# Kernel optimization log

Measured on AMD Instinct MI355X. Metric: run time of the kernel, lower is better.

## Reference

```python
import jax, jax.numpy as jnp
import numpy as np

N_PIECES = 20  # hard-coded in FSEncoderSized.__init__ (FSPool(..., 20))


def conv1x1(x, w, b):
    # x: (B, Cin, N), w: (Cout, Cin), b: (Cout,) -> (B, Cout, N)
    return jnp.einsum('bcn,dc->bdn', x, w) + b[None, :, None]


def fspool(x, weight):
    # x: (B, C, N); weight: (C, N_PIECES+1)
    # FSPool with n=None: sizes = arange(N)/(N-1) clamped to 1, mask all ones.
    B, C, N = x.shape
    ratio = jnp.clip(jnp.arange(N, dtype=jnp.float32) / max(N - 1, 1), 0.0, 1.0)
    pos = N_PIECES * ratio                      # (N,) in [0, N_PIECES]
    idx = jnp.floor(pos).astype(jnp.int32)
    frac = pos - idx
    left = weight[:, idx]                       # (C, N)
    right = weight[:, jnp.clip(idx + 1, 0, N_PIECES)]
    w = (1.0 - frac)[None, :] * left + frac[None, :] * right  # (C, N)
    xs = -jnp.sort(-x, axis=2)                  # descending sort along set dim
    return jnp.sum(xs * w[None], axis=2)        # (B, C)


def setup_inputs() -> dict:
    key = jax.random.key(0)
    ks = jax.random.split(key, 12)
    B, Cin, N = 1024, 5, 512
    dim, Cout = 256, 129
    C = Cout - 1  # 128
    x = jax.random.normal(ks[0], (B, Cin, N), dtype=jnp.float32)
    mask = (jax.random.uniform(ks[1], (B, N)) < 0.8).astype(jnp.float32)

    def kaiming(k, co, ci):
        return jax.random.normal(k, (co, ci), dtype=jnp.float32) * np.sqrt(2.0 / ci)

    w1 = kaiming(ks[2], dim, Cin); b1 = jnp.zeros((dim,), jnp.float32)
    w2 = kaiming(ks[3], dim, dim); b2 = jnp.zeros((dim,), jnp.float32)
    w3 = kaiming(ks[4], dim, dim); b3 = jnp.zeros((dim,), jnp.float32)
    w4 = kaiming(ks[5], C, dim);   b4 = jnp.zeros((C,), jnp.float32)
    pool_w = jax.random.normal(ks[6], (C, N_PIECES + 1), dtype=jnp.float32) * 0.1
    return {'x': x, 'mask': mask, 'w1': w1, 'b1': b1, 'w2': w2, 'b2': b2,
            'w3': w3, 'b3': b3, 'w4': w4, 'b4': b4, 'pool_w': pool_w}


def reference(x, mask, w1, b1, w2, b2, w3, b3, w4, b4, pool_w):
    m = mask[:, None, :]                         # (B, 1, N)
    h = jax.nn.relu(conv1x1(x, w1, b1))
    h = jax.nn.relu(conv1x1(h, w2, b2))
    h = jax.nn.relu(conv1x1(h, w3, b3))
    h = conv1x1(h, w4, b4)                       # (B, C, N)
    h = h / h.shape[2]                           # x / x.size(2)
    h = h * m
    pooled = fspool(h, pool_w)                   # (B, C)
    size_feat = jnp.mean(m, axis=2) * 4.0        # (B, 1)
    return jnp.concatenate([pooled, size_feat], axis=1)  # (B, C+1)
```

## Files before the change

### kernel.cpp

```cpp
#include <hip/hip_runtime.h>
#include <hip/hip_bf16.h>

typedef __bf16 bf16x8 __attribute__((ext_vector_type(8)));
typedef float f32x4 __attribute__((ext_vector_type(4)));
typedef unsigned short ushort_t;

#define NPOS 512
#define CIN  5
#define CO   128

static __device__ __forceinline__ unsigned short f2bf(float f){
  union { __hip_bfloat16 h; unsigned short u; } cv;
  cv.h = __float2bfloat16(f);
  return cv.u;
}

static __device__ __forceinline__ unsigned cvtpk_u32(float a, float b){
  union { __hip_bfloat162 h2; unsigned u; } cv;
  cv.h2 = __float22bfloat162_rn(make_float2(a, b));
  return cv.u;
}

static __device__ __forceinline__ unsigned pk_min_u16(unsigned a, unsigned b){
  unsigned d; asm("v_pk_min_u16 %0, %1, %2" : "=v"(d) : "v"(a), "v"(b)); return d;
}
static __device__ __forceinline__ unsigned pk_max_u16(unsigned a, unsigned b){
  unsigned d; asm("v_pk_max_u16 %0, %1, %2" : "=v"(d) : "v"(a), "v"(b)); return d;
}
static __device__ __forceinline__ unsigned pk_max_i16(unsigned a, unsigned b){
  unsigned d; asm("v_pk_max_i16 %0, %1, %2" : "=v"(d) : "v"(a), "v"(b)); return d;
}

template<int CTRL>
static __device__ __forceinline__ unsigned mov_dpp_u32(unsigned v){
  return (unsigned)__builtin_amdgcn_mov_dpp((int)v, CTRL, 0xf, 0xf, true);
}
template<int CTRL>
static __device__ __forceinline__ float fadd_dpp(float s){
  union {float f; int i;} u; u.f = s;
  union {int i; float f;} q; q.i = __builtin_amdgcn_mov_dpp(u.i, CTRL, 0xf, 0xf, true);
  return s + q.f;
}

__global__ void k_prep(const float* __restrict__ w1, const float* __restrict__ w2,
                       const float* __restrict__ w3, const float* __restrict__ w4,
                       const float* __restrict__ pw,
                       ushort_t* __restrict__ o, float* __restrict__ Wt){
  int i = blockIdx.x*256 + threadIdx.x;
  if (i < 65536)        o[i] = f2bf(w2[i]);
  else if (i < 131072)  o[i] = f2bf(w3[i-65536]);
  else if (i < 163840)  o[i] = f2bf(w4[i-131072]);
  else if (i < 172032){
    int j = i - 163840;
    int d = j >> 5, k = j & 31;
    o[i] = (k < CIN) ? f2bf(w1[d*CIN + k]) : (ushort_t)0;
  } else {
    int j = i - 172032;
    int c = j >> 9, ii = j & 511;
    int rk = 511 - ii;
    float pos = (float)rk * (20.0f/511.0f);
    int idx = (int)pos; if (idx > 20) idx = 20;
    float frac = pos - (float)idx;
    int i2 = (idx+1 > 20) ? 20 : idx+1;
    float wl = pw[c*21 + idx], wr = pw[c*21 + i2];
    Wt[c*512 + ii] = wl + frac*(wr - wl);
  }
}


template<int NSD, int KSTR>
static __device__ __forceinline__ void preload_w(bf16x8 (&wr)[3][4],
    const ushort_t* __restrict__ Wb, int slot, int ks, int wave, int lane){
  const int m = lane & 15, quad = lane >> 4;
  const int d0 = wave * (NSD*16);
  #pragma unroll
  for (int sd=0; sd<NSD; sd++)
    wr[slot][sd] = *(const bf16x8*)(Wb + (d0 + sd*16 + m)*KSTR + ks*32 + quad*8);
}

template<int NKS>
static __device__ __forceinline__ void mfma_WA(bf16x8 (&wr)[3][4],
    const ushort_t* __restrict__ Wb,
    const ushort_t* __restrict__ A0, const ushort_t* __restrict__ A1,
    const float* __restrict__ bias,
    f32x4 (&c0)[4][4], f32x4 (&c1)[4][4], int wave, int lane){
  const int quad = lane >> 4;
  f32x4 bvv[4];
  #pragma unroll
  for (int db=0; db<4; db++){
    float4 b4v = *(const float4*)(bias + wave*64 + db*16 + quad*4);
    bvv[db] = (f32x4){b4v.x, b4v.y, b4v.z, b4v.w};
  }
  #pragma unroll
  for (int ks=0; ks<NKS; ks++){
    if (ks+2 < NKS) preload_w<4,256>(wr, Wb, (ks+2)%3, ks+2, wave, lane);
    bf16x8 a0[4], a1[4];
    #pragma unroll
    for (int nb=0; nb<4; nb++){
      a0[nb] = *(const bf16x8*)(A0 + ((nb*512 + ks*64 + lane) << 3));
      a1[nb] = *(const bf16x8*)(A1 + ((nb*512 + ks*64 + lane) << 3));
    }
    #pragma unroll
    for (int db=0; db<4; db++){
      #pragma unroll
      for (int nb=0; nb<4; nb++){
        if (ks == 0){
          c0[nb][db] = __builtin_amdgcn_mfma_f32_16x16x32_bf16(wr[0][db], a0[nb], bvv[db], 0,0,0);
          c1[nb][db] = __builtin_amdgcn_mfma_f32_16x16x32_bf16(wr[0][db], a1[nb], bvv[db], 0,0,0);
        } else {
          c0[nb][db] = __builtin_amdgcn_mfma_f32_16x16x32_bf16(wr[ks%3][db], a0[nb], c0[nb][db], 0,0,0);
          c1[nb][db] = __builtin_amdgcn_mfma_f32_16x16x32_bf16(wr[ks%3][db], a1[nb], c1[nb][db], 0,0,0);
        }
      }
    }
  }
}

static __device__ __forceinline__ void mfma_L4(bf16x8 (&wr)[3][4],
    const ushort_t* __restrict__ Wb,
    const ushort_t* __restrict__ A0, const ushort_t* __restrict__ A1,
    const float* __restrict__ bias,
    f32x4 (&c0)[4][4], f32x4 (&c1)[4][4], int wave, int lane){
  const int m = lane & 15;
  f32x4 bvv[2];
  #pragma unroll
  for (int sd=0; sd<2; sd++){
    float bv = bias[wave*32 + sd*16 + m];
    bvv[sd] = (f32x4){bv,bv,bv,bv};
  }
  #pragma unroll
  for (int ks=0; ks<8; ks++){
    if (ks+2 < 8) preload_w<2,256>(wr, Wb, (ks+2)%3, ks+2, wave, lane);
    bf16x8 a0[4], a1[4];
    #pragma unroll
    for (int sn=0; sn<4; sn++){
      a0[sn] = *(const bf16x8*)(A0 + ((sn*512 + ks*64 + lane) << 3));
      a1[sn] = *(const bf16x8*)(A1 + ((sn*512 + ks*64 + lane) << 3));
    }
    #pragma unroll
    for (int sd=0; sd<2; sd++){
      #pragma unroll
      for (int sn=0; sn<4; sn++){
        if (ks == 0){
          c0[sn][sd] = __builtin_amdgcn_mfma_f32_16x16x32_bf16(a0[sn], wr[0][sd], bvv[sd], 0,0,0);
          c1[sn][sd] = __builtin_amdgcn_mfma_f32_16x16x32_bf16(a1[sn], wr[0][sd], bvv[sd], 0,0,0);
        } else {
          c0[sn][sd] = __builtin_amdgcn_mfma_f32_16x16x32_bf16(a0[sn], wr[ks%3][sd], c0[sn][sd], 0,0,0);
          c1[sn][sd] = __builtin_amdgcn_mfma_f32_16x16x32_bf16(a1[sn], wr[ks%3][sd], c1[sn][sd], 0,0,0);
        }
      }
    }
  }
}

static __device__ __forceinline__ void epilogue_relu(const f32x4 (&c)[4][4],
    ushort_t* __restrict__ dst, int wave, int lane){
  const int m = lane & 15, quad = lane >> 4;
  #pragma unroll
  for (int db=0; db<4; db++){
    int cb    = wave*64 + db*16 + quad*4;
    int colpt = (cb>>5)*64 + ((cb>>3)&3)*16;
    int half  = (quad & 1) ? 4 : 0;
    #pragma unroll
    for (int nb=0; nb<4; nb++){
      unsigned u01 = pk_max_i16(cvtpk_u32(c[nb][db][0], c[nb][db][1]), 0u);
      unsigned u23 = pk_max_i16(cvtpk_u32(c[nb][db][2], c[nb][db][3]), 0u);
      int chunk = nb*512 + colpt + m;
      *(uint2*)&dst[(chunk << 3) + half] = make_uint2(u01, u23);
    }
  }
}

__global__ __launch_bounds__(256,2) void k_fused(
  const float* __restrict__ x, const float* __restrict__ mask,
  const ushort_t* __restrict__ w1b, const float* __restrict__ b1,
  const ushort_t* __restrict__ w2b, const float* __restrict__ b2,
  const ushort_t* __restrict__ w3b, const float* __restrict__ b3,
  const ushort_t* __restrict__ w4b, const float* __restrict__ b4,
  ushort_t* __restrict__ h4)
{
  __shared__ __align__(16) ushort_t Act0[64*256];
  __shared__ __align__(16) ushort_t Act1[64*256];
  const int t    = threadIdx.x;
  const int bid  = blockIdx.x;
  const int b    = bid >> 2;
  const int n0   = (bid & 3) << 7;
  const int wave = t >> 6, lane = t & 63;

  bf16x8 wr[3][4];
  f32x4  c0[4][4], c1[4][4];

  {
    const int sn = t >> 6, col = (t >> 4) & 3, n16 = t & 15;
    uint4 u0 = make_uint4(0u,0u,0u,0u), u1 = u0;
    if (col == 0){
      const float* xp = x + (size_t)b*CIN*NPOS + n0 + sn*16 + n16;
      u0.x = cvtpk_u32(xp[0],      xp[NPOS]);
      u0.y = cvtpk_u32(xp[2*NPOS], xp[3*NPOS]);
      u0.z = cvtpk_u32(xp[4*NPOS], 0.f);
      const float* xq = xp + 64;
      u1.x = cvtpk_u32(xq[0],      xq[NPOS]);
      u1.y = cvtpk_u32(xq[2*NPOS], xq[3*NPOS]);
      u1.z = cvtpk_u32(xq[4*NPOS], 0.f);
    }
    *(uint4*)&Act0[(sn*512 + col*16 + n16) << 3] = u0;
    *(uint4*)&Act1[(sn*512 + col*16 + n16) << 3] = u1;
  }
  preload_w<4,32>(wr, w1b, 0, 0, wave, lane);
  __syncthreads();

  mfma_WA<1>(wr, w1b, Act0, Act1, b1, c0, c1, wave, lane);
  __syncthreads();
  preload_w<4,256>(wr, w2b, 0, 0, wave, lane);
  preload_w<4,256>(wr, w2b, 1, 1, wave, lane);
  epilogue_relu(c0, Act0, wave, lane);
  epilogue_relu(c1, Act1, wave, lane);
  __syncthreads();

  mfma_WA<8>(wr, w2b, Act0, Act1, b2, c0, c1, wave, lane);
  __syncthreads();
  preload_w<4,256>(wr, w3b, 0, 0, wave, lane);
  preload_w<4,256>(wr, w3b, 1, 1, wave, lane);
  epilogue_relu(c0, Act0, wave, lane);
  epilogue_relu(c1, Act1, wave, lane);
  __syncthreads();

  mfma_WA<8>(wr, w3b, Act0, Act1, b3, c0, c1, wave, lane);
  __syncthreads();
  preload_w<2,256>(wr, w4b, 0, 0, wave, lane);
  preload_w<2,256>(wr, w4b, 1, 1, wave, lane);
  epilogue_relu(c0, Act0, wave, lane);
  epilogue_relu(c1, Act1, wave, lane);
  __syncthreads();

  mfma_L4(wr, w4b, Act0, Act1, b4, c0, c1, wave, lane);
  {
    const int m = lane & 15, quad = lane >> 4;
    const float* mk = mask + (size_t)b*NPOS + n0;
    #pragma unroll
    for (int sd=0;sd<2;sd++){
      const int d = wave*32 + sd*16 + m;
      ushort_t* rowp = h4 + ((size_t)b*CO + d)*NPOS + n0;
      #pragma unroll
      for (int sn=0;sn<4;sn++){
        float4 mr0 = *(const float4*)(mk + sn*16 + quad*4);
        float4 mr1 = *(const float4*)(mk + 64 + sn*16 + quad*4);
        unsigned q0 = cvtpk_u32(c0[sn][sd][0] * (1.0f/512.0f) * mr0.x,
                                c0[sn][sd][1] * (1.0f/512.0f) * mr0.y);
        unsigned q1 = cvtpk_u32(c0[sn][sd][2] * (1.0f/512.0f) * mr0.z,
                                c0[sn][sd][3] * (1.0f/512.0f) * mr0.w);
        *(uint2*)(rowp + sn*16 + quad*4) = make_uint2(q0, q1);
        unsigned p0 = cvtpk_u32(c1[sn][sd][0] * (1.0f/512.0f) * mr1.x,
                                c1[sn][sd][1] * (1.0f/512.0f) * mr1.y);
        unsigned p1 = cvtpk_u32(c1[sn][sd][2] * (1.0f/512.0f) * mr1.z,
                                c1[sn][sd][3] * (1.0f/512.0f) * mr1.w);
        *(uint2*)(rowp + 64 + sn*16 + quad*4) = make_uint2(p0, p1);
      }
    }
  }
}


static __device__ __forceinline__ void ce_up(unsigned &a, unsigned &b){
  unsigned mn = pk_min_u16(a,b), mx = pk_max_u16(a,b); a = mn; b = mx;
}
static __device__ __forceinline__ void ce_dn(unsigned &a, unsigned &b){
  unsigned mn = pk_min_u16(a,b), mx = pk_max_u16(a,b); a = mx; b = mn;
}
static __device__ __forceinline__ void clean8(unsigned (&v)[8]){
  ce_up(v[0],v[4]); ce_up(v[1],v[5]); ce_up(v[2],v[6]); ce_up(v[3],v[7]);
  ce_up(v[0],v[2]); ce_up(v[1],v[3]); ce_up(v[4],v[6]); ce_up(v[5],v[7]);
  ce_up(v[0],v[1]); ce_up(v[2],v[3]); ce_up(v[4],v[5]); ce_up(v[6],v[7]);
}
static __device__ __forceinline__ void flip8(unsigned (&v)[8], unsigned f){
  #pragma unroll
  for (int i=0;i<8;i++) v[i] ^= f;
}
template<int CTRL>
static __device__ __forceinline__ void xr_dpp(unsigned (&v)[8], bool low){
  #pragma unroll
  for (int i=0;i<8;i++){
    unsigned p = mov_dpp_u32<CTRL>(v[i]);
    unsigned mn = pk_min_u16(v[i], p), mx = pk_max_u16(v[i], p);
    v[i] = low ? mn : mx;
  }
}
static __device__ __forceinline__ void xr_shfl(unsigned (&v)[8], int lm, bool low){
  #pragma unroll
  for (int i=0;i<8;i++){
    unsigned p = (unsigned)__shfl_xor((int)v[i], lm);
    unsigned mn = pk_min_u16(v[i], p), mx = pk_max_u16(v[i], p);
    v[i] = low ? mn : mx;
  }
}

__global__ void k_pool(const ushort_t* __restrict__ h4, const float* __restrict__ Wt,
                       const float* __restrict__ mask, float* __restrict__ out)
{
  const int lane = threadIdx.x & 63;
  const int wave = threadIdx.x >> 6;
  const size_t r0 = (size_t)blockIdx.x*8 + wave*2;
  const int b0 = (int)(r0 >> 7), c0 = (int)(r0 & 127);
  const int b1_ = (int)((r0+1) >> 7), c1 = (int)((r0+1) & 127);

  uint4 ra = *(const uint4*)(h4 + r0*NPOS     + lane*8);
  uint4 rb = *(const uint4*)(h4 + (r0+1)*NPOS + lane*8);

  float w0[8], w1a[8];
  *(float4*)&w0[0]  = *(const float4*)(Wt + c0*512 + lane*8);
  *(float4*)&w0[4]  = *(const float4*)(Wt + c0*512 + lane*8 + 4);
  *(float4*)&w1a[0] = *(const float4*)(Wt + c1*512 + lane*8);
  *(float4*)&w1a[4] = *(const float4*)(Wt + c1*512 + lane*8 + 4);

  unsigned v[8];
  v[0] = (ra.x & 0xFFFFu) | (rb.x << 16);
  v[1] = (ra.x >> 16)     | (rb.x & 0xFFFF0000u);
  v[2] = (ra.y & 0xFFFFu) | (rb.y << 16);
  v[3] = (ra.y >> 16)     | (rb.y & 0xFFFF0000u);
  v[4] = (ra.z & 0xFFFFu) | (rb.z << 16);
  v[5] = (ra.z >> 16)     | (rb.z & 0xFFFF0000u);
  v[6] = (ra.w & 0xFFFFu) | (rb.w << 16);
  v[7] = (ra.w >> 16)     | (rb.w & 0xFFFF0000u);

  #pragma unroll
  for (int i=0;i<8;i++){
    unsigned sb = (v[i] >> 15) & 0x00010001u;
    v[i] = v[i] ^ 0x80008000u ^ (sb * 0x7FFFu);
  }

  const bool lo1  = (lane & 1)  == 0;
  const bool lo2  = (lane & 2)  == 0;
  const bool lo4  = (lane & 4)  == 0;
  const bool lo8  = (lane & 8)  == 0;
  const bool lo16 = (lane & 16) == 0;
  const bool lo32 = (lane & 32) == 0;

  const unsigned F8   = (lane & 1)  ? 0xFFFFFFFFu : 0u;
  const unsigned F16  = (lane & 2)  ? 0xFFFFFFFFu : 0u;
  const unsigned F32  = (lane & 4)  ? 0xFFFFFFFFu : 0u;
  const unsigned F64  = (lane & 8)  ? 0xFFFFFFFFu : 0u;
  const unsigned F128 = (lane & 16) ? 0xFFFFFFFFu : 0u;
  const unsigned F256 = (lane & 32) ? 0xFFFFFFFFu : 0u;

  ce_up(v[0],v[1]); ce_dn(v[2],v[3]); ce_up(v[4],v[5]); ce_dn(v[6],v[7]);
  ce_up(v[0],v[2]); ce_up(v[1],v[3]); ce_dn(v[4],v[6]); ce_dn(v[5],v[7]);
  ce_up(v[0],v[1]); ce_up(v[2],v[3]); ce_dn(v[4],v[5]); ce_dn(v[6],v[7]);

  flip8(v, F8);
  clean8(v);
  flip8(v, F8 ^ F16);
  xr_dpp<0xB1>(v, lo1);
  clean8(v);
  flip8(v, F16 ^ F32);
  xr_dpp<0x4E>(v, lo2); xr_dpp<0xB1>(v, lo1);
  clean8(v);
  flip8(v, F32 ^ F64);
  xr_shfl(v, 4, lo4); xr_dpp<0x4E>(v, lo2); xr_dpp<0xB1>(v, lo1);
  clean8(v);
  flip8(v, F64 ^ F128);
  xr_dpp<0x128>(v, lo8); xr_shfl(v, 4, lo4); xr_dpp<0x4E>(v, lo2); xr_dpp<0xB1>(v, lo1);
  clean8(v);
  flip8(v, F128 ^ F256);
  xr_shfl(v, 16, lo16); xr_dpp<0x128>(v, lo8); xr_shfl(v, 4, lo4);
  xr_dpp<0x4E>(v, lo2); xr_dpp<0xB1>(v, lo1);
  clean8(v);
  flip8(v, F256);
  xr_shfl(v, 32, lo32); xr_shfl(v, 16, lo16); xr_dpp<0x128>(v, lo8);
  xr_shfl(v, 4, lo4); xr_dpp<0x4E>(v, lo2); xr_dpp<0xB1>(v, lo1);
  clean8(v);

  #pragma unroll
  for (int i=0;i<8;i++){
    unsigned sb = ((~v[i]) >> 15) & 0x00010001u;
    v[i] = v[i] ^ 0x80008000u ^ (sb * 0x7FFFu);
  }

  float s0 = 0.f, s1 = 0.f;
  #pragma unroll
  for (int i=0;i<8;i++){
    union {unsigned u; float f;} lo, hi;
    lo.u = v[i] << 16;
    hi.u = v[i] & 0xFFFF0000u;
    s0 = fmaf(lo.f, w0[i],  s0);
    s1 = fmaf(hi.f, w1a[i], s1);
  }
  s0 = fadd_dpp<0xB1>(s0);  s1 = fadd_dpp<0xB1>(s1);
  s0 = fadd_dpp<0x4E>(s0);  s1 = fadd_dpp<0x4E>(s1);
  s0 = fadd_dpp<0x128>(s0); s1 = fadd_dpp<0x128>(s1);
  s0 += __shfl_xor(s0, 4);  s1 += __shfl_xor(s1, 4);
  s0 += __shfl_xor(s0, 16); s1 += __shfl_xor(s1, 16);
  s0 += __shfl_xor(s0, 32); s1 += __shfl_xor(s1, 32);

  if (lane == 0){
    out[b0*129 + c0]  = s0;
    out[b1_*129 + c1] = s1;
  }

  if (blockIdx.x < 1024 && wave == 0){
    const int b = blockIdx.x;
    float s = 0.f;
    #pragma unroll
    for (int i=0;i<2;i++){
      float4 mv = *(const float4*)(mask + (size_t)b*NPOS + lane*8 + i*4);
      s += mv.x + mv.y + mv.z + mv.w;
    }
    s = fadd_dpp<0xB1>(s); s = fadd_dpp<0x4E>(s); s = fadd_dpp<0x128>(s);
    s += __shfl_xor(s, 4); s += __shfl_xor(s, 16); s += __shfl_xor(s, 32);
    if (lane == 0) out[b*129 + 128] = s * (1.0f/128.0f);
  }
}

extern "C" void kernel_launch(void* const* d_in, const int* in_sizes, int n_in,
                              void* d_out, int out_size, void* d_ws, size_t ws_size,
                              hipStream_t stream){
  const float* x    = (const float*)d_in[0];
  const float* mask = (const float*)d_in[1];
  const float* w1   = (const float*)d_in[2];
  const float* b1   = (const float*)d_in[3];
  const float* w2   = (const float*)d_in[4];
  const float* b2   = (const float*)d_in[5];
  const float* w3   = (const float*)d_in[6];
  const float* b3   = (const float*)d_in[7];
  const float* w4   = (const float*)d_in[8];
  const float* b4   = (const float*)d_in[9];
  const float* pw   = (const float*)d_in[10];
  float* out = (float*)d_out;

  ushort_t* h4  = (ushort_t*)d_ws;
  ushort_t* w2b = h4 + (size_t)1024*CO*NPOS;
  ushort_t* w3b = w2b + 65536;
  ushort_t* w4b = w3b + 65536;
  ushort_t* w1b = w4b + 32768;
  float*    Wt  = (float*)(w1b + 8192);

  k_prep <<<928,   256, 0, stream>>>(w1, w2, w3, w4, pw, w2b, Wt);
  k_fused<<<4096,  256, 0, stream>>>(x, mask, w1b, b1, w2b, b2, w3b, b3, w4b, b4, h4);
  k_pool <<<16384, 256, 0, stream>>>(h4, Wt, mask, out);
}
```

Measured before the change: 385.2 us.

## Fuse pooling into MLP kernel via last-arriving-block atomic counter

Removes the separate pooling kernel. Each of the four blocks per batch row signals completion through an atomic counter, and the last block to arrive runs the sort-and-weighted-sum pooling for all 128 channels of that row, while h4 is likely still in L2. The 1/512 scale is folded into the w4 and b4 weights during prep, and the counters are zeroed in prep. In exchange, pooling now runs on only 1024 blocks in the tail instead of 16384, which risks poorer parallelism and a serialized tail.

```diff
diff --git a/kernel.cpp b/kernel.cpp
--- a/kernel.cpp
+++ b/kernel.cpp
@@ -44,17 +44,19 @@
 
 __global__ void k_prep(const float* __restrict__ w1, const float* __restrict__ w2,
                        const float* __restrict__ w3, const float* __restrict__ w4,
-                       const float* __restrict__ pw,
-                       ushort_t* __restrict__ o, float* __restrict__ Wt){
+                       const float* __restrict__ pw, const float* __restrict__ b4,
+                       ushort_t* __restrict__ o, float* __restrict__ Wt,
+                       float* __restrict__ b4s, unsigned* __restrict__ cnt){
   int i = blockIdx.x*256 + threadIdx.x;
+  if (i < 1024) cnt[i] = 0u;
   if (i < 65536)        o[i] = f2bf(w2[i]);
   else if (i < 131072)  o[i] = f2bf(w3[i-65536]);
-  else if (i < 163840)  o[i] = f2bf(w4[i-131072]);
+  else if (i < 163840)  o[i] = f2bf(w4[i-131072] * (1.0f/512.0f));
   else if (i < 172032){
     int j = i - 163840;
     int d = j >> 5, k = j & 31;
     o[i] = (k < CIN) ? f2bf(w1[d*CIN + k]) : (ushort_t)0;
-  } else {
+  } else if (i < 237568){
     int j = i - 172032;
     int c = j >> 9, ii = j & 511;
     int rk = 511 - ii;
@@ -64,9 +66,10 @@
     int i2 = (idx+1 > 20) ? 20 : idx+1;
     float wl = pw[c*21 + idx], wr = pw[c*21 + i2];
     Wt[c*512 + ii] = wl + frac*(wr - wl);
-  }
-}
-
+  } else if (i < 237696){
+    b4s[i-237568] = b4[i-237568] * (1.0f/512.0f);
+  }
+}
 
 template<int NSD, int KSTR>
 static __device__ __forceinline__ void preload_w(bf16x8 (&wr)[3][4],
@@ -171,16 +174,147 @@
   }
 }
 
-__global__ __launch_bounds__(256,2) void k_fused(
+static __device__ __forceinline__ void ce_up(unsigned &a, unsigned &b){
+  unsigned mn = pk_min_u16(a,b), mx = pk_max_u16(a,b); a = mn; b = mx;
+}
+static __device__ __forceinline__ void ce_dn(unsigned &a, unsigned &b){
+  unsigned mn = pk_min_u16(a,b), mx = pk_max_u16(a,b); a = mx; b = mn;
+}
+static __device__ __forceinline__ void clean8(unsigned (&v)[8]){
+  ce_up(v[0],v[4]); ce_up(v[1],v[5]); ce_up(v[2],v[6]); ce_up(v[3],v[7]);
+  ce_up(v[0],v[2]); ce_up(v[1],v[3]); ce_up(v[4],v[6]); ce_up(v[5],v[7]);
+  ce_up(v[0],v[1]); ce_up(v[2],v[3]); ce_up(v[4],v[5]); ce_up(v[6],v[7]);
+}
+static __device__ __forceinline__ void flip8(unsigned (&v)[8], unsigned f){
+  #pragma unroll
+  for (int i=0;i<8;i++) v[i] ^= f;
+}
+template<int CTRL>
+static __device__ __forceinline__ void xr_dpp(unsigned (&v)[8], bool low){
+  #pragma unroll
+  for (int i=0;i<8;i++){
+    unsigned p = mov_dpp_u32<CTRL>(v[i]);
+    unsigned mn = pk_min_u16(v[i], p), mx = pk_max_u16(v[i], p);
+    v[i] = low ? mn : mx;
+  }
+}
+static __device__ __forceinline__ void xr_shfl(unsigned (&v)[8], int lm, bool low){
+  #pragma unroll
+  for (int i=0;i<8;i++){
+    unsigned p = (unsigned)__shfl_xor((int)v[i], lm);
+    unsigned mn = pk_min_u16(v[i], p), mx = pk_max_u16(v[i], p);
+    v[i] = low ? mn : mx;
+  }
+}
+
+static __device__ __forceinline__ void pool2(const ushort_t* __restrict__ rowp,
+    const float* __restrict__ Wt, float* __restrict__ out, int b, int c0, int lane){
+  uint4 ra = *(const uint4*)(rowp + lane*8);
+  uint4 rb = *(const uint4*)(rowp + NPOS + lane*8);
+
+  unsigned v[8];
+  v[0] = (ra.x & 0xFFFFu) | (rb.x << 16);
+  v[1] = (ra.x >> 16)     | (rb.x & 0xFFFF0000u);
+  v[2] = (ra.y & 0xFFFFu) | (rb.y << 16);
+  v[3] = (ra.y >> 16)     | (rb.y & 0xFFFF0000u);
+  v[4] = (ra.z & 0xFFFFu) | (rb.z << 16);
+  v[5] = (ra.z >> 16)     | (rb.z & 0xFFFF0000u);
+  v[6] = (ra.w & 0xFFFFu) | (rb.w << 16);
+  v[7] = (ra.w >> 16)     | (rb.w & 0xFFFF0000u);
+
+  #pragma unroll
+  for (int i=0;i<8;i++){
+    unsigned sb = (v[i] >> 15) & 0x00010001u;
+    v[i] = v[i] ^ 0x80008000u ^ (sb * 0x7FFFu);
+  }
+
+  const bool lo1  = (lane & 1)  == 0;
+  const bool lo2  = (lane & 2)  == 0;
+  const bool lo4  = (lane & 4)  == 0;
+  const bool lo8  = (lane & 8)  == 0;
+  const bool lo16 = (lane & 16) == 0;
+  const bool lo32 = (lane & 32) == 0;
+
+  const unsigned F8   = (lane & 1)  ? 0xFFFFFFFFu : 0u;
+  const unsigned F16  = (lane & 2)  ? 0xFFFFFFFFu : 0u;
+  const unsigned F32  = (lane & 4)  ? 0xFFFFFFFFu : 0u;
+  const unsigned F64  = (lane & 8)  ? 0xFFFFFFFFu : 0u;
+  const unsigned F128 = (lane & 16) ? 0xFFFFFFFFu : 0u;
+  const unsigned F256 = (lane & 32) ? 0xFFFFFFFFu : 0u;
+
+  ce_up(v[0],v[1]); ce_dn(v[2],v[3]); ce_up(v[4],v[5]); ce_dn(v[6],v[7]);
+  ce_up(v[0],v[2]); ce_up(v[1],v[3]); ce_dn(v[4],v[6]); ce_dn(v[5],v[7]);
+  ce_up(v[0],v[1]); ce_up(v[2],v[3]); ce_dn(v[4],v[5]); ce_dn(v[6],v[7]);
+
+  flip8(v, F8);
+  clean8(v);
+  flip8(v, F8 ^ F16);
+  xr_dpp<0xB1>(v, lo1);
+  clean8(v);
+  flip8(v, F16 ^ F32);
+  xr_dpp<0x4E>(v, lo2); xr_dpp<0xB1>(v, lo1);
+  clean8(v);
+  flip8(v, F32 ^ F64);
+  xr_shfl(v, 4, lo4); xr_dpp<0x4E>(v, lo2); xr_dpp<0xB1>(v, lo1);
+  clean8(v);
+  flip8(v, F64 ^ F128);
+  xr_dpp<0x128>(v, lo8); xr_shfl(v, 4, lo4); xr_dpp<0x4E>(v, lo2); xr_dpp<0xB1>(v, lo1);
+  clean8(v);
+  flip8(v, F128 ^ F256);
+  xr_shfl(v, 16, lo16); xr_dpp<0x128>(v, lo8); xr_shfl(v, 4, lo4);
+  xr_dpp<0x4E>(v, lo2); xr_dpp<0xB1>(v, lo1);
+  clean8(v);
+  flip8(v, F256);
+  xr_shfl(v, 32, lo32); xr_shfl(v, 16, lo16); xr_dpp<0x128>(v, lo8);
+  xr_shfl(v, 4, lo4); xr_dpp<0x4E>(v, lo2); xr_dpp<0xB1>(v, lo1);
+  clean8(v);
+
+  #pragma unroll
+  for (int i=0;i<8;i++){
+    unsigned sb = ((~v[i]) >> 15) & 0x00010001u;
+    v[i] = v[i] ^ 0x80008000u ^ (sb * 0x7FFFu);
+  }
+
+  float w0[8], w1a[8];
+  *(float4*)&w0[0]  = *(const float4*)(Wt + c0*512 + lane*8);
+  *(float4*)&w0[4]  = *(const float4*)(Wt + c0*512 + lane*8 + 4);
+  *(float4*)&w1a[0] = *(const float4*)(Wt + (c0+1)*512 + lane*8);
+  *(float4*)&w1a[4] = *(const float4*)(Wt + (c0+1)*512 + lane*8 + 4);
+
+  float s0 = 0.f, s1 = 0.f;
+  #pragma unroll
+  for (int i=0;i<8;i++){
+    union {unsigned u; float f;} lo, hi;
+    lo.u = v[i] << 16;
+    hi.u = v[i] & 0xFFFF0000u;
+    s0 = fmaf(lo.f, w0[i],  s0);
+    s1 = fmaf(hi.f, w1a[i], s1);
+  }
+  s0 = fadd_dpp<0xB1>(s0);  s1 = fadd_dpp<0xB1>(s1);
+  s0 = fadd_dpp<0x4E>(s0);  s1 = fadd_dpp<0x4E>(s1);
+  s0 = fadd_dpp<0x128>(s0); s1 = fadd_dpp<0x128>(s1);
+  s0 += __shfl_xor(s0, 4);  s1 += __shfl_xor(s1, 4);
+  s0 += __shfl_xor(s0, 16); s1 += __shfl_xor(s1, 16);
+  s0 += __shfl_xor(s0, 32); s1 += __shfl_xor(s1, 32);
+
+  if (lane == 0){
+    out[b*129 + c0]     = s0;
+    out[b*129 + c0 + 1] = s1;
+  }
+}
+
+__global__ __launch_bounds__(256,2) void k_mega(
   const float* __restrict__ x, const float* __restrict__ mask,
   const ushort_t* __restrict__ w1b, const float* __restrict__ b1,
   const ushort_t* __restrict__ w2b, const float* __restrict__ b2,
   const ushort_t* __restrict__ w3b, const float* __restrict__ b3,
-  const ushort_t* __restrict__ w4b, const float* __restrict__ b4,
-  ushort_t* __restrict__ h4)
+  const ushort_t* __restrict__ w4b, const float* __restrict__ b4s,
+  ushort_t* __restrict__ h4, unsigned* __restrict__ cnt,
+  const float* __restrict__ Wt, float* __restrict__ out)
 {
   __shared__ __align__(16) ushort_t Act0[64*256];
   __shared__ __align__(16) ushort_t Act1[64*256];
+  __shared__ unsigned pflag;
   const int t    = threadIdx.x;
   const int bid  = blockIdx.x;
   const int b    = bid >> 2;
@@ -233,7 +367,7 @@
   epilogue_relu(c1, Act1, wave, lane);
   __syncthreads();
 
-  mfma_L4(wr, w4b, Act0, Act1, b4, c0, c1, wave, lane);
+  mfma_L4(wr, w4b, Act0, Act1, b4s, c0, c1, wave, lane);
   {
     const int m = lane & 15, quad = lane >> 4;
     const float* mk = mask + (size_t)b*NPOS + n0;
@@ -245,159 +379,31 @@
       for (int sn=0;sn<4;sn++){
         float4 mr0 = *(const float4*)(mk + sn*16 + quad*4);
         float4 mr1 = *(const float4*)(mk + 64 + sn*16 + quad*4);
-        unsigned q0 = cvtpk_u32(c0[sn][sd][0] * (1.0f/512.0f) * mr0.x,
-                                c0[sn][sd][1] * (1.0f/512.0f) * mr0.y);
-        unsigned q1 = cvtpk_u32(c0[sn][sd][2] * (1.0f/512.0f) * mr0.z,
-                                c0[sn][sd][3] * (1.0f/512.0f) * mr0.w);
+        unsigned q0 = cvtpk_u32(c0[sn][sd][0] * mr0.x, c0[sn][sd][1] * mr0.y);
+        unsigned q1 = cvtpk_u32(c0[sn][sd][2] * mr0.z, c0[sn][sd][3] * mr0.w);
         *(uint2*)(rowp + sn*16 + quad*4) = make_uint2(q0, q1);
-        unsigned p0 = cvtpk_u32(c1[sn][sd][0] * (1.0f/512.0f) * mr1.x,
-                                c1[sn][sd][1] * (1.0f/512.0f) * mr1.y);
-        unsigned p1 = cvtpk_u32(c1[sn][sd][2] * (1.0f/512.0f) * mr1.z,
-                                c1[sn][sd][3] * (1.0f/512.0f) * mr1.w);
+        unsigned p0 = cvtpk_u32(c1[sn][sd][0] * mr1.x, c1[sn][sd][1] * mr1.y);
+        unsigned p1 = cvtpk_u32(c1[sn][sd][2] * mr1.z, c1[sn][sd][3] * mr1.w);
         *(uint2*)(rowp + 64 + sn*16 + quad*4) = make_uint2(p0, p1);
       }
     }
   }
-}
-
-
-static __device__ __forceinline__ void ce_up(unsigned &a, unsigned &b){
-  unsigned mn = pk_min_u16(a,b), mx = pk_max_u16(a,b); a = mn; b = mx;
-}
-static __device__ __forceinline__ void ce_dn(unsigned &a, unsigned &b){
-  unsigned mn = pk_min_u16(a,b), mx = pk_max_u16(a,b); a = mx; b = mn;
-}
-static __device__ __forceinline__ void clean8(unsigned (&v)[8]){
-  ce_up(v[0],v[4]); ce_up(v[1],v[5]); ce_up(v[2],v[6]); ce_up(v[3],v[7]);
-  ce_up(v[0],v[2]); ce_up(v[1],v[3]); ce_up(v[4],v[6]); ce_up(v[5],v[7]);
-  ce_up(v[0],v[1]); ce_up(v[2],v[3]); ce_up(v[4],v[5]); ce_up(v[6],v[7]);
-}
-static __device__ __forceinline__ void flip8(unsigned (&v)[8], unsigned f){
-  #pragma unroll
-  for (int i=0;i<8;i++) v[i] ^= f;
-}
-template<int CTRL>
-static __device__ __forceinline__ void xr_dpp(unsigned (&v)[8], bool low){
-  #pragma unroll
-  for (int i=0;i<8;i++){
-    unsigned p = mov_dpp_u32<CTRL>(v[i]);
-    unsigned mn = pk_min_u16(v[i], p), mx = pk_max_u16(v[i], p);
-    v[i] = low ? mn : mx;
-  }
-}
-static __device__ __forceinline__ void xr_shfl(unsigned (&v)[8], int lm, bool low){
-  #pragma unroll
-  for (int i=0;i<8;i++){
-    unsigned p = (unsigned)__shfl_xor((int)v[i], lm);
-    unsigned mn = pk_min_u16(v[i], p), mx = pk_max_u16(v[i], p);
-    v[i] = low ? mn : mx;
-  }
-}
-
-__global__ void k_pool(const ushort_t* __restrict__ h4, const float* __restrict__ Wt,
-                       const float* __restrict__ mask, float* __restrict__ out)
-{
-  const int lane = threadIdx.x & 63;
-  const int wave = threadIdx.x >> 6;
-  const size_t r0 = (size_t)blockIdx.x*8 + wave*2;
-  const int b0 = (int)(r0 >> 7), c0 = (int)(r0 & 127);
-  const int b1_ = (int)((r0+1) >> 7), c1 = (int)((r0+1) & 127);
-
-  uint4 ra = *(const uint4*)(h4 + r0*NPOS     + lane*8);
-  uint4 rb = *(const uint4*)(h4 + (r0+1)*NPOS + lane*8);
-
-  float w0[8], w1a[8];
-  *(float4*)&w0[0]  = *(const float4*)(Wt + c0*512 + lane*8);
-  *(float4*)&w0[4]  = *(const float4*)(Wt + c0*512 + lane*8 + 4);
-  *(float4*)&w1a[0] = *(const float4*)(Wt + c1*512 + lane*8);
-  *(float4*)&w1a[4] = *(const float4*)(Wt + c1*512 + lane*8 + 4);
-
-  unsigned v[8];
-  v[0] = (ra.x & 0xFFFFu) | (rb.x << 16);
-  v[1] = (ra.x >> 16)     | (rb.x & 0xFFFF0000u);
-  v[2] = (ra.y & 0xFFFFu) | (rb.y << 16);
-  v[3] = (ra.y >> 16)     | (rb.y & 0xFFFF0000u);
-  v[4] = (ra.z & 0xFFFFu) | (rb.z << 16);
-  v[5] = (ra.z >> 16)     | (rb.z & 0xFFFF0000u);
-  v[6] = (ra.w & 0xFFFFu) | (rb.w << 16);
-  v[7] = (ra.w >> 16)     | (rb.w & 0xFFFF0000u);
-
-  #pragma unroll
-  for (int i=0;i<8;i++){
-    unsigned sb = (v[i] >> 15) & 0x00010001u;
-    v[i] = v[i] ^ 0x80008000u ^ (sb * 0x7FFFu);
-  }
-
-  const bool lo1  = (lane & 1)  == 0;
-  const bool lo2  = (lane & 2)  == 0;
-  const bool lo4  = (lane & 4)  == 0;
-  const bool lo8  = (lane & 8)  == 0;
-  const bool lo16 = (lane & 16) == 0;
-  const bool lo32 = (lane & 32) == 0;
-
-  const unsigned F8   = (lane & 1)  ? 0xFFFFFFFFu : 0u;
-  const unsigned F16  = (lane & 2)  ? 0xFFFFFFFFu : 0u;
-  const unsigned F32  = (lane & 4)  ? 0xFFFFFFFFu : 0u;
-  const unsigned F64  = (lane & 8)  ? 0xFFFFFFFFu : 0u;
-  const unsigned F128 = (lane & 16) ? 0xFFFFFFFFu : 0u;
-  const unsigned F256 = (lane & 32) ? 0xFFFFFFFFu : 0u;
-
-  ce_up(v[0],v[1]); ce_dn(v[2],v[3]); ce_up(v[4],v[5]); ce_dn(v[6],v[7]);
-  ce_up(v[0],v[2]); ce_up(v[1],v[3]); ce_dn(v[4],v[6]); ce_dn(v[5],v[7]);
-  ce_up(v[0],v[1]); ce_up(v[2],v[3]); ce_dn(v[4],v[5]); ce_dn(v[6],v[7]);
-
-  flip8(v, F8);
-  clean8(v);
-  flip8(v, F8 ^ F16);
-  xr_dpp<0xB1>(v, lo1);
-  clean8(v);
-  flip8(v, F16 ^ F32);
-  xr_dpp<0x4E>(v, lo2); xr_dpp<0xB1>(v, lo1);
-  clean8(v);
-  flip8(v, F32 ^ F64);
-  xr_shfl(v, 4, lo4); xr_dpp<0x4E>(v, lo2); xr_dpp<0xB1>(v, lo1);
-  clean8(v);
-  flip8(v, F64 ^ F128);
-  xr_dpp<0x128>(v, lo8); xr_shfl(v, 4, lo4); xr_dpp<0x4E>(v, lo2); xr_dpp<0xB1>(v, lo1);
-  clean8(v);
-  flip8(v, F128 ^ F256);
-  xr_shfl(v, 16, lo16); xr_dpp<0x128>(v, lo8); xr_shfl(v, 4, lo4);
-  xr_dpp<0x4E>(v, lo2); xr_dpp<0xB1>(v, lo1);
-  clean8(v);
-  flip8(v, F256);
-  xr_shfl(v, 32, lo32); xr_shfl(v, 16, lo16); xr_dpp<0x128>(v, lo8);
-  xr_shfl(v, 4, lo4); xr_dpp<0x4E>(v, lo2); xr_dpp<0xB1>(v, lo1);
-  clean8(v);
-
-  #pragma unroll
-  for (int i=0;i<8;i++){
-    unsigned sb = ((~v[i]) >> 15) & 0x00010001u;
-    v[i] = v[i] ^ 0x80008000u ^ (sb * 0x7FFFu);
-  }
-
-  float s0 = 0.f, s1 = 0.f;
-  #pragma unroll
-  for (int i=0;i<8;i++){
-    union {unsigned u; float f;} lo, hi;
-    lo.u = v[i] << 16;
-    hi.u = v[i] & 0xFFFF0000u;
-    s0 = fmaf(lo.f, w0[i],  s0);
-    s1 = fmaf(hi.f, w1a[i], s1);
-  }
-  s0 = fadd_dpp<0xB1>(s0);  s1 = fadd_dpp<0xB1>(s1);
-  s0 = fadd_dpp<0x4E>(s0);  s1 = fadd_dpp<0x4E>(s1);
-  s0 = fadd_dpp<0x128>(s0); s1 = fadd_dpp<0x128>(s1);
-  s0 += __shfl_xor(s0, 4);  s1 += __shfl_xor(s1, 4);
-  s0 += __shfl_xor(s0, 16); s1 += __shfl_xor(s1, 16);
-  s0 += __shfl_xor(s0, 32); s1 += __shfl_xor(s1, 32);
-
-  if (lane == 0){
-    out[b0*129 + c0]  = s0;
-    out[b1_*129 + c1] = s1;
-  }
-
-  if (blockIdx.x < 1024 && wave == 0){
-    const int b = blockIdx.x;
+
+  __threadfence();
+  __syncthreads();
+  if (t == 0)
+    pflag = __hip_atomic_fetch_add(&cnt[b], 1u, __ATOMIC_ACQ_REL, __HIP_MEMORY_SCOPE_AGENT);
+  __syncthreads();
+  if (pflag != 3u) return;
+
+  const ushort_t* hb = h4 + (size_t)b*CO*NPOS;
+  #pragma unroll 1
+  for (int iter=0; iter<16; iter++){
+    int cc = iter*8 + wave*2;
+    pool2(hb + (size_t)cc*NPOS, Wt, out, b, cc, lane);
+  }
+
+  if (wave == 0){
     float s = 0.f;
     #pragma unroll
     for (int i=0;i<2;i++){
@@ -432,8 +438,10 @@
   ushort_t* w4b = w3b + 65536;
   ushort_t* w1b = w4b + 32768;
   float*    Wt  = (float*)(w1b + 8192);
-
-  k_prep <<<928,   256, 0, stream>>>(w1, w2, w3, w4, pw, w2b, Wt);
-  k_fused<<<4096,  256, 0, stream>>>(x, mask, w1b, b1, w2b, b2, w3b, b3, w4b, b4, h4);
-  k_pool <<<16384, 256, 0, stream>>>(h4, Wt, mask, out);
-}
+  float*    b4s = Wt + 65536;
+  unsigned* cnt = (unsigned*)(b4s + 128);
+
+  k_prep <<<929,  256, 0, stream>>>(w1, w2, w3, w4, pw, b4, w2b, Wt, b4s, cnt);
+  k_mega <<<4096, 256, 0, stream>>>(x, mask, w1b, b1, w2b, b2, w3b, b3, w4b, b4s,
+                                    h4, cnt, Wt, out);
+}
```

Measured after the change: 1.215 ms. +215.4%, slower.
